# Kernel tuning notes

Measured on AMD Instinct MI355X. Metric: run time of the kernel, lower is better.

## Reference

```python
import jax, jax.numpy as jnp
import numpy as np

N_NODES = 100000
N_EDGES = 400000
IN_F, HID, OUT_F = 128, 1024, 64


def gcn_conv(x, src, dst, ew, W, b, n):
    # PyG GCNConv: add self-loops (weight 1), symmetric normalization,
    # out[dst] += norm * (x @ W)[src], then bias.
    loop = jnp.arange(n)
    s = jnp.concatenate([src, loop])
    d = jnp.concatenate([dst, loop])
    w = jnp.concatenate([ew, jnp.ones((n,), dtype=ew.dtype)])
    deg = jax.ops.segment_sum(w, d, num_segments=n)
    dinv = jnp.where(deg > 0, jax.lax.rsqrt(deg), 0.0)
    norm = dinv[s] * w * dinv[d]                      # [E+N]
    h = x @ W                                         # [N, out]
    out = jax.ops.segment_sum(h[s] * norm[:, None], d, num_segments=n)
    return out + b


def setup_inputs() -> dict:
    key = jax.random.key(0)
    k = jax.random.split(key, 8)
    x = jax.random.normal(k[0], (N_NODES, IN_F), dtype=jnp.float32)
    edge_index = jax.random.randint(k[1], (2, N_EDGES), 0, N_NODES, dtype=jnp.int64)
    edge_weight = jax.random.uniform(k[2], (N_EDGES,), dtype=jnp.float32)
    # Glorot-ish init for params
    W1 = jax.random.normal(k[3], (IN_F, HID), dtype=jnp.float32) * (1.0 / np.sqrt(IN_F))
    b1 = jnp.zeros((HID,), dtype=jnp.float32)
    W2 = jax.random.normal(k[4], (HID, OUT_F), dtype=jnp.float32) * (1.0 / np.sqrt(HID))
    b2 = jnp.zeros((OUT_F,), dtype=jnp.float32)
    return {"x": x, "edge_index": edge_index, "edge_weight": edge_weight,
            "W1": W1, "b1": b1, "W2": W2, "b2": b2}


def reference(x, edge_index, edge_weight, W1, b1, W2, b2):
    src, dst = edge_index[0], edge_index[1]
    h = gcn_conv(x, src, dst, edge_weight, W1, b1, N_NODES)
    h = jax.nn.relu(h)
    # F.dropout with training=False is identity (eval mode)
    out = gcn_conv(h, src, dst, edge_weight, W2, b2, N_NODES)
    return out
```

## Files before the change

kernel.cpp:

```cpp
#include <hip/hip_runtime.h>
#include <hip/hip_bf16.h>

#define N_NODES 100000
#define N_EDGES 400000
#define IN_F    128
#define HID     1024
#define OUT_F   64
#define BUCKET_CAP 24

typedef __attribute__((ext_vector_type(8))) short short8;
typedef __attribute__((ext_vector_type(4))) float floatx4;

__device__ inline unsigned short f2bf(float f) {
    unsigned int u = __float_as_uint(f);
    unsigned int r = u + 0x7FFF + ((u >> 16) & 1);
    return (unsigned short)(r >> 16);
}

__device__ inline unsigned int cvtpk(float a, float b) {
    union { __hip_bfloat162 h; unsigned int u; } v;
    v.h = __float22bfloat162_rn(float2{a, b});
    return v.u;
}

__device__ inline float bf2f(unsigned int lo16) {
    return __uint_as_float(lo16 << 16);
}

__device__ __forceinline__ void gload_lds16(const void* g, void* l) {
    __builtin_amdgcn_global_load_lds(
        (const __attribute__((address_space(1))) void*)g,
        (__attribute__((address_space(3))) void*)l, 16, 0, 0);
}

#define XB_BLOCKS  6250
#define WSB_BLOCKS 768
#define DEG_BLOCKS 1563

__global__ __launch_bounds__(256) void setup_kernel(
    const float* __restrict__ x, unsigned short* __restrict__ xb,
    const float* __restrict__ W1, const float* __restrict__ W2,
    unsigned short* __restrict__ S,
    const int* __restrict__ dst, const float* __restrict__ ew,
    float* __restrict__ deg)
{
    int b = blockIdx.x;
    int tid = threadIdx.x;
    if (b < XB_BLOCKS) {
        long i = (long)b * 256 + tid;
        float4 a = ((const float4*)x)[i * 2];
        float4 c = ((const float4*)x)[i * 2 + 1];
        ((uint4*)xb)[i] = make_uint4(cvtpk(a.x, a.y), cvtpk(a.z, a.w),
                                     cvtpk(c.x, c.y), cvtpk(c.z, c.w));
    } else if (b < XB_BLOCKS + WSB_BLOCKS) {
        int idx = b - XB_BLOCKS;
        int c = idx / 48;
        int r = (idx % 48) * 256 + tid;
        int f = r >> 9;
        int l = (r >> 3) & 63;
        int j = r & 7;
        float v;
        if (f < 16) {
            int nt = f >> 2, kt = f & 3;
            int hid = c * 64 + nt * 16 + (l & 15);
            int k   = kt * 32 + (l >> 4) * 8 + j;
            v = W1[(long)k * HID + hid];
        } else {
            int f2 = f - 16;
            int kb = f2 >> 2, nt2 = f2 & 3;
            int kh = c * 64 + kb * 32 + (j >> 2) * 16 + (l >> 4) * 4 + (j & 3);
            int oc = nt2 * 16 + (l & 15);
            v = W2[(long)kh * OUT_F + oc];
        }
        S[(long)c * 12288 + r] = f2bf(v);
    } else {
        int e = (b - XB_BLOCKS - WSB_BLOCKS) * 256 + tid;
        if (e < N_EDGES) atomicAdd(&deg[dst[e]], ew[e]);
    }
}

__global__ void fill_pairs_kernel(const int* __restrict__ src, const int* __restrict__ dst,
                                  const float* __restrict__ w, const float* __restrict__ deg,
                                  int* __restrict__ cnt, int2* __restrict__ pairs, int E) {
    int e = blockIdx.x * blockDim.x + threadIdx.x;
    if (e < E) {
        int s = src[e];
        int d = dst[e];
        float nv = rsqrtf(deg[s] + 1.0f) * w[e] * rsqrtf(deg[d] + 1.0f);
        int slot = atomicAdd(&cnt[d], 1);
        if (slot < BUCKET_CAP)
            pairs[(long)d * BUCKET_CAP + slot] = make_int2(s, __float_as_int(nv));
    }
}

__global__ __launch_bounds__(256) void gather64_kernel(
    const int2* __restrict__ pairs, const int* __restrict__ cnt,
    const float* __restrict__ deg, const unsigned short* __restrict__ tb,
    const float* __restrict__ bias, float* __restrict__ out)
{
    int node = blockIdx.x * 16 + (threadIdx.x >> 4);
    int l = threadIdx.x & 15;
    float di = rsqrtf(deg[node] + 1.0f);
    float s = di * di;
    uint2 tv = ((const uint2*)(tb + (long)node * OUT_F))[l];
    float4 bb = ((const float4*)bias)[l];
    float4 acc;
    acc.x = bf2f(tv.x & 0xffffu) * s + bb.x;
    acc.y = bf2f(tv.x >> 16) * s + bb.y;
    acc.z = bf2f(tv.y & 0xffffu) * s + bb.z;
    acc.w = bf2f(tv.y >> 16) * s + bb.w;
    int c = cnt[node]; c = c < BUCKET_CAP ? c : BUCKET_CAP;
    const int2* p = pairs + (long)node * BUCKET_CAP;
    int j = 0;
    for (; j + 4 <= c; j += 4) {
        int4 q01 = *(const int4*)(p + j);
        int4 q23 = *(const int4*)(p + j + 2);
        uint2 u0 = ((const uint2*)(tb + (long)q01.x * OUT_F))[l];
        uint2 u1 = ((const uint2*)(tb + (long)q01.z * OUT_F))[l];
        uint2 u2 = ((const uint2*)(tb + (long)q23.x * OUT_F))[l];
        uint2 u3 = ((const uint2*)(tb + (long)q23.z * OUT_F))[l];
        float n0 = __int_as_float(q01.y), n1 = __int_as_float(q01.w);
        float n2 = __int_as_float(q23.y), n3 = __int_as_float(q23.w);
        acc.x += n0 * bf2f(u0.x & 0xffffu) + n1 * bf2f(u1.x & 0xffffu)
               + n2 * bf2f(u2.x & 0xffffu) + n3 * bf2f(u3.x & 0xffffu);
        acc.y += n0 * bf2f(u0.x >> 16) + n1 * bf2f(u1.x >> 16)
               + n2 * bf2f(u2.x >> 16) + n3 * bf2f(u3.x >> 16);
        acc.z += n0 * bf2f(u0.y & 0xffffu) + n1 * bf2f(u1.y & 0xffffu)
               + n2 * bf2f(u2.y & 0xffffu) + n3 * bf2f(u3.y & 0xffffu);
        acc.w += n0 * bf2f(u0.y >> 16) + n1 * bf2f(u1.y >> 16)
               + n2 * bf2f(u2.y >> 16) + n3 * bf2f(u3.y >> 16);
    }
    for (; j < c; j++) {
        int2 pp = p[j];
        float nv = __int_as_float(pp.y);
        uint2 u = ((const uint2*)(tb + (long)pp.x * OUT_F))[l];
        acc.x += nv * bf2f(u.x & 0xffffu);
        acc.y += nv * bf2f(u.x >> 16);
        acc.z += nv * bf2f(u.y & 0xffffu);
        acc.w += nv * bf2f(u.y >> 16);
    }
    ((float4*)(out + (long)node * OUT_F))[l] = acc;
}


__global__ __launch_bounds__(512, 2) void fused_mlp_mfma_kernel(
    const int2* __restrict__ pairs, const int* __restrict__ cnt,
    const float* __restrict__ deg, const unsigned short* __restrict__ xb,
    const unsigned short* __restrict__ Wstream,
    const float* __restrict__ b1, unsigned short* __restrict__ Tb, int M)
{
    __shared__ unsigned short Wbuf[2][12288];

    const int tid = threadIdx.x;
    const int w   = tid >> 6;
    const int l   = tid & 63;
    const int lr  = l & 15;
    const int lq  = l >> 4;
    const long row0 = (long)blockIdx.x * 256 + w * 32;

    {
        const unsigned short* g = Wstream + (long)(w * 3) * 512 + l * 8;
        unsigned short* d = &Wbuf[0][(w * 3) * 512];
        #pragma unroll
        for (int s = 0; s < 3; s++)
            gload_lds16(g + s * 512, d + s * 512);
    }

    short8 bx[2][4];
    #pragma unroll
    for (int rt = 0; rt < 2; rt++) {
        long row = row0 + rt * 16 + lr;
        if (row < M) {
            float facc[4][8];
            float di = rsqrtf(deg[row] + 1.0f);
            float s = di * di;
            const uint4* xrow = (const uint4*)(xb + row * IN_F);
            #pragma unroll
            for (int kt = 0; kt < 4; kt++) {
                uint4 u = xrow[kt * 4 + lq];
                facc[kt][0] = bf2f(u.x & 0xffffu) * s; facc[kt][1] = bf2f(u.x >> 16) * s;
                facc[kt][2] = bf2f(u.y & 0xffffu) * s; facc[kt][3] = bf2f(u.y >> 16) * s;
                facc[kt][4] = bf2f(u.z & 0xffffu) * s; facc[kt][5] = bf2f(u.z >> 16) * s;
                facc[kt][6] = bf2f(u.w & 0xffffu) * s; facc[kt][7] = bf2f(u.w >> 16) * s;
            }
            int c = cnt[row]; c = c < BUCKET_CAP ? c : BUCKET_CAP;
            const int2* p = pairs + (long)row * BUCKET_CAP;
            for (int j = 0; j < c; j++) {
                int2 pp = p[j];
                float nv = __int_as_float(pp.y);
                const uint4* srow = (const uint4*)(xb + (long)pp.x * IN_F);
                #pragma unroll
                for (int kt = 0; kt < 4; kt++) {
                    uint4 u = srow[kt * 4 + lq];
                    facc[kt][0] += nv * bf2f(u.x & 0xffffu); facc[kt][1] += nv * bf2f(u.x >> 16);
                    facc[kt][2] += nv * bf2f(u.y & 0xffffu); facc[kt][3] += nv * bf2f(u.y >> 16);
                    facc[kt][4] += nv * bf2f(u.z & 0xffffu); facc[kt][5] += nv * bf2f(u.z >> 16);
                    facc[kt][6] += nv * bf2f(u.w & 0xffffu); facc[kt][7] += nv * bf2f(u.w >> 16);
                }
            }
            #pragma unroll
            for (int kt = 0; kt < 4; kt++)
                #pragma unroll
                for (int i = 0; i < 8; i++)
                    bx[rt][kt][i] = (short)f2bf(facc[kt][i]);
        } else {
            #pragma unroll
            for (int kt = 0; kt < 4; kt++)
                #pragma unroll
                for (int i = 0; i < 8; i++)
                    bx[rt][kt][i] = 0;
        }
    }

    __syncthreads();

    floatx4 tacc[2][4];
    #pragma unroll
    for (int rt = 0; rt < 2; rt++)
        #pragma unroll
        for (int nt = 0; nt < 4; nt++)
            tacc[rt][nt] = (floatx4)0.0f;

    for (int c = 0; c < 16; c++) {
        const unsigned short* Wb = &Wbuf[c & 1][0];

        if (c < 15) {
            const unsigned short* g = Wstream + (long)(c + 1) * 12288 + (long)(w * 3) * 512 + l * 8;
            unsigned short* d = &Wbuf[(c + 1) & 1][(w * 3) * 512];
            #pragma unroll
            for (int s = 0; s < 3; s++)
                gload_lds16(g + s * 512, d + s * 512);
        }

        #pragma unroll
        for (int h = 0; h < 2; h++) {
            floatx4 hacc[2][2];
            #pragma unroll
            for (int rt = 0; rt < 2; rt++)
                #pragma unroll
                for (int n = 0; n < 2; n++)
                    hacc[rt][n] = (floatx4)0.0f;

            #pragma unroll
            for (int n = 0; n < 2; n++) {
                const int nt = h * 2 + n;
                short8 w1f[4];
                #pragma unroll
                for (int kt = 0; kt < 4; kt++)
                    w1f[kt] = *(const short8*)(Wb + (nt * 4 + kt) * 512 + l * 8);
                #pragma unroll
                for (int kt = 0; kt < 4; kt++) {
                    hacc[0][n] = __builtin_amdgcn_mfma_f32_16x16x32_bf16(w1f[kt], bx[0][kt], hacc[0][n], 0, 0, 0);
                    hacc[1][n] = __builtin_amdgcn_mfma_f32_16x16x32_bf16(w1f[kt], bx[1][kt], hacc[1][n], 0, 0, 0);
                }
            }

            floatx4 bb0 = *(const floatx4*)(b1 + c * 64 + (h * 2 + 0) * 16 + lq * 4);
            floatx4 bb1 = *(const floatx4*)(b1 + c * 64 + (h * 2 + 1) * 16 + lq * 4);
            short8 hf[2];
            #pragma unroll
            for (int rt = 0; rt < 2; rt++) {
                #pragma unroll
                for (int r = 0; r < 4; r++) {
                    hf[rt][r]     = (short)f2bf(fmaxf(hacc[rt][0][r] + bb0[r], 0.0f));
                    hf[rt][r + 4] = (short)f2bf(fmaxf(hacc[rt][1][r] + bb1[r], 0.0f));
                }
            }

            #pragma unroll
            for (int nt2 = 0; nt2 < 4; nt2++) {
                short8 w2f = *(const short8*)(Wb + (16 + h * 4 + nt2) * 512 + l * 8);
                tacc[0][nt2] = __builtin_amdgcn_mfma_f32_16x16x32_bf16(w2f, hf[0], tacc[0][nt2], 0, 0, 0);
                tacc[1][nt2] = __builtin_amdgcn_mfma_f32_16x16x32_bf16(w2f, hf[1], tacc[1][nt2], 0, 0, 0);
            }
        }

        if (c < 15) __syncthreads();
    }

    #pragma unroll
    for (int rt = 0; rt < 2; rt++) {
        long row = row0 + rt * 16 + lr;
        if (row < M) {
            #pragma unroll
            for (int nt = 0; nt < 4; nt++) {
                unsigned int q0 = (unsigned int)f2bf(tacc[rt][nt][0]) | ((unsigned int)f2bf(tacc[rt][nt][1]) << 16);
                unsigned int q1 = (unsigned int)f2bf(tacc[rt][nt][2]) | ((unsigned int)f2bf(tacc[rt][nt][3]) << 16);
                *(uint2*)(Tb + row * OUT_F + nt * 16 + lq * 4) = make_uint2(q0, q1);
            }
        }
    }
}


extern "C" void kernel_launch(void* const* d_in, const int* in_sizes, int n_in,
                              void* d_out, int out_size, void* d_ws, size_t ws_size,
                              hipStream_t stream) {
    const float* x   = (const float*)d_in[0];
    const int*   src = (const int*)d_in[1];
    const int*   dst = ((const int*)d_in[1]) + N_EDGES;
    const float* ew  = (const float*)d_in[2];
    const float* W1  = (const float*)d_in[3];
    const float* b1  = (const float*)d_in[4];
    const float* W2  = (const float*)d_in[5];
    const float* b2  = (const float*)d_in[6];
    float* out = (float*)d_out;

    float* ws     = (float*)d_ws;
    float* deg    = ws;
    int*   cnt    = (int*)(ws + 100096);
    int2*  pairs  = (int2*)(ws + 200192);
    unsigned short* xb  = (unsigned short*)(ws + 5000192);
    unsigned short* tb  = (unsigned short*)(ws + 11400192);
    unsigned short* wstream = (unsigned short*)(ws + 14600192);

    const int B = 256;

    hipMemsetAsync(ws, 0, 200192 * sizeof(float), stream);

    setup_kernel<<<XB_BLOCKS + WSB_BLOCKS + DEG_BLOCKS, B, 0, stream>>>(
        x, xb, W1, W2, wstream, dst, ew, deg);

    fill_pairs_kernel<<<(N_EDGES + B - 1) / B, B, 0, stream>>>(src, dst, ew, deg, cnt, pairs, N_EDGES);

    fused_mlp_mfma_kernel<<<(N_NODES + 255) / 256, 512, 0, stream>>>(
        pairs, cnt, deg, xb, wstream, b1, tb, N_NODES);

    gather64_kernel<<<N_NODES / 16, 256, 0, stream>>>(pairs, cnt, deg, tb, b2, out);
}
```

Measured before the change: 152.4 us.

## Fold edge bucketing into setup kernel and apply degree normalization at gather time

```diff
diff --git a/kernel.cpp b/kernel.cpp
--- a/kernel.cpp
+++ b/kernel.cpp
@@ -33,16 +33,18 @@
         (__attribute__((address_space(3))) void*)l, 16, 0, 0);
 }
 
-#define XB_BLOCKS  6250
-#define WSB_BLOCKS 768
-#define DEG_BLOCKS 1563
+#define XB_BLOCKS   6250
+#define WSB_BLOCKS  768
+#define DEG_BLOCKS  1563
+#define PAIR_BLOCKS 1563
 
 __global__ __launch_bounds__(256) void setup_kernel(
     const float* __restrict__ x, unsigned short* __restrict__ xb,
     const float* __restrict__ W1, const float* __restrict__ W2,
     unsigned short* __restrict__ S,
-    const int* __restrict__ dst, const float* __restrict__ ew,
-    float* __restrict__ deg)
+    const int* __restrict__ src, const int* __restrict__ dst,
+    const float* __restrict__ ew,
+    float* __restrict__ deg, int* __restrict__ cnt, int2* __restrict__ pairs)
 {
     int b = blockIdx.x;
     int tid = threadIdx.x;
@@ -73,23 +75,18 @@
             v = W2[(long)kh * OUT_F + oc];
         }
         S[(long)c * 12288 + r] = f2bf(v);
-    } else {
+    } else if (b < XB_BLOCKS + WSB_BLOCKS + DEG_BLOCKS) {
         int e = (b - XB_BLOCKS - WSB_BLOCKS) * 256 + tid;
         if (e < N_EDGES) atomicAdd(&deg[dst[e]], ew[e]);
-    }
-}
-
-__global__ void fill_pairs_kernel(const int* __restrict__ src, const int* __restrict__ dst,
-                                  const float* __restrict__ w, const float* __restrict__ deg,
-                                  int* __restrict__ cnt, int2* __restrict__ pairs, int E) {
-    int e = blockIdx.x * blockDim.x + threadIdx.x;
-    if (e < E) {
-        int s = src[e];
-        int d = dst[e];
-        float nv = rsqrtf(deg[s] + 1.0f) * w[e] * rsqrtf(deg[d] + 1.0f);
-        int slot = atomicAdd(&cnt[d], 1);
-        if (slot < BUCKET_CAP)
-            pairs[(long)d * BUCKET_CAP + slot] = make_int2(s, __float_as_int(nv));
+    } else {
+        int e = (b - XB_BLOCKS - WSB_BLOCKS - DEG_BLOCKS) * 256 + tid;
+        if (e < N_EDGES) {
+            int s = src[e];
+            int d = dst[e];
+            int slot = atomicAdd(&cnt[d], 1);
+            if (slot < BUCKET_CAP)
+                pairs[(long)d * BUCKET_CAP + slot] = make_int2(s, __float_as_int(ew[e]));
+        }
     }
 }
 
@@ -115,12 +112,15 @@
     for (; j + 4 <= c; j += 4) {
         int4 q01 = *(const int4*)(p + j);
         int4 q23 = *(const int4*)(p + j + 2);
+        float g0 = deg[q01.x], g1 = deg[q01.z], g2 = deg[q23.x], g3 = deg[q23.z];
         uint2 u0 = ((const uint2*)(tb + (long)q01.x * OUT_F))[l];
         uint2 u1 = ((const uint2*)(tb + (long)q01.z * OUT_F))[l];
         uint2 u2 = ((const uint2*)(tb + (long)q23.x * OUT_F))[l];
         uint2 u3 = ((const uint2*)(tb + (long)q23.z * OUT_F))[l];
-        float n0 = __int_as_float(q01.y), n1 = __int_as_float(q01.w);
-        float n2 = __int_as_float(q23.y), n3 = __int_as_float(q23.w);
+        float n0 = rsqrtf(g0 + 1.0f) * __int_as_float(q01.y) * di;
+        float n1 = rsqrtf(g1 + 1.0f) * __int_as_float(q01.w) * di;
+        float n2 = rsqrtf(g2 + 1.0f) * __int_as_float(q23.y) * di;
+        float n3 = rsqrtf(g3 + 1.0f) * __int_as_float(q23.w) * di;
         acc.x += n0 * bf2f(u0.x & 0xffffu) + n1 * bf2f(u1.x & 0xffffu)
                + n2 * bf2f(u2.x & 0xffffu) + n3 * bf2f(u3.x & 0xffffu);
         acc.y += n0 * bf2f(u0.x >> 16) + n1 * bf2f(u1.x >> 16)
@@ -132,7 +132,7 @@
     }
     for (; j < c; j++) {
         int2 pp = p[j];
-        float nv = __int_as_float(pp.y);
+        float nv = rsqrtf(deg[pp.x] + 1.0f) * __int_as_float(pp.y) * di;
         uint2 u = ((const uint2*)(tb + (long)pp.x * OUT_F))[l];
         acc.x += nv * bf2f(u.x & 0xffffu);
         acc.y += nv * bf2f(u.x >> 16);
@@ -187,7 +187,7 @@
             const int2* p = pairs + (long)row * BUCKET_CAP;
             for (int j = 0; j < c; j++) {
                 int2 pp = p[j];
-                float nv = __int_as_float(pp.y);
+                float nv = rsqrtf(deg[pp.x] + 1.0f) * __int_as_float(pp.y) * di;
                 const uint4* srow = (const uint4*)(xb + (long)pp.x * IN_F);
                 #pragma unroll
                 for (int kt = 0; kt < 4; kt++) {
@@ -318,10 +318,8 @@
 
     hipMemsetAsync(ws, 0, 200192 * sizeof(float), stream);
 
-    setup_kernel<<<XB_BLOCKS + WSB_BLOCKS + DEG_BLOCKS, B, 0, stream>>>(
-        x, xb, W1, W2, wstream, dst, ew, deg);
-
-    fill_pairs_kernel<<<(N_EDGES + B - 1) / B, B, 0, stream>>>(src, dst, ew, deg, cnt, pairs, N_EDGES);
+    setup_kernel<<<XB_BLOCKS + WSB_BLOCKS + DEG_BLOCKS + PAIR_BLOCKS, B, 0, stream>>>(
+        x, xb, W1, W2, wstream, src, dst, ew, deg, cnt, pairs);
 
     fused_mlp_mfma_kernel<<<(N_NODES + 255) / 256, 512, 0, stream>>>(
         pairs, cnt, deg, xb, wstream, b1, tb, N_NODES);
```

New measurement: 155.7 us. 1.02x slower.
